# Optimization experiments

Hardware: AMD Instinct MI355X
Metric: run time of the kernel (lower is better)

## Reference

```python
import jax, jax.numpy as jnp
import numpy as np
import math

CHUNK = 64

def _linear(x, W, b):
    # torch nn.Linear: y = x @ W.T + b
    return jnp.einsum('bsd,ed->bse', x, W) + b

def setup_inputs() -> dict:
    key = jax.random.key(0)
    ks = jax.random.split(key, 10)
    B, S, D = 4, 4096, 512
    scale = 0.02
    inp = {
        'x': jax.random.normal(ks[0], (B, S, D), jnp.float32),
        'base_phases': jax.random.normal(ks[1], (S, D), jnp.float32) * math.pi,
        'Wk': jax.random.normal(ks[2], (D, D), jnp.float32) * scale,
        'bk': jnp.zeros((D,), jnp.float32),
        'Wv': jax.random.normal(ks[3], (D, D), jnp.float32) * scale,
        'bv': jnp.zeros((D,), jnp.float32),
        'Wq': jax.random.normal(ks[4], (D, D), jnp.float32) * scale,
        'bq': jnp.zeros((D,), jnp.float32),
        'Wkm': jax.random.normal(ks[5], (D, D), jnp.float32) * scale,
        'bkm': jnp.zeros((D,), jnp.float32),
        'Wqm': jax.random.normal(ks[6], (D, D), jnp.float32) * scale,
        'bqm': jnp.zeros((D,), jnp.float32),
        'mod_scale': jnp.ones((1,), jnp.float32) * 0.1,
        'ln_g': jnp.ones((D,), jnp.float32),
        'ln_b': jnp.zeros((D,), jnp.float32),
        'Wo': jax.random.normal(ks[7], (D, D), jnp.float32) * scale,
        'bo': jnp.zeros((D,), jnp.float32),
    }
    return inp

def reference(x, base_phases, Wk, bk, Wv, bv, Wq, bq, Wkm, bkm, Wqm, bqm, mod_scale, ln_g, ln_b, Wo, bo):
    B, S, D = x.shape
    bp = base_phases[:S][None]                      # [1,S,D]
    key = _linear(x, Wk, bk)
    value = _linear(x, Wv, bv)
    query = _linear(x, Wq, bq)
    key_phase = bp + _linear(key, Wkm, bkm) * mod_scale
    query_phase = bp + _linear(query, Wqm, bqm) * mod_scale
    bound_real = value * jnp.cos(key_phase)
    bound_imag = value * jnp.sin(key_phase)
    # chunked cumulative memory (S divisible by CHUNK -> no padding)
    nC = S // CHUNK
    br = bound_real.reshape(B, nC, CHUNK, D)
    bi = bound_imag.reshape(B, nC, CHUNK, D)
    qp = query_phase.reshape(B, nC, CHUNK, D)
    mem_real = jnp.cumsum(br, axis=2)
    mem_imag = jnp.cumsum(bi, axis=2)
    retrieved = (mem_real * jnp.cos(qp) + mem_imag * jnp.sin(qp)).reshape(B, S, D)
    retrieved = retrieved / math.sqrt(D)
    # LayerNorm + Linear (to_out)
    mu = jnp.mean(retrieved, axis=-1, keepdims=True)
    var = jnp.mean((retrieved - mu) ** 2, axis=-1, keepdims=True)
    normed = (retrieved - mu) / jnp.sqrt(var + 1e-5) * ln_g + ln_b
    out = _linear(normed, Wo, bo)
    return x + out
```

## Files before the change

### kernel.cpp

```cpp
#include <hip/hip_runtime.h>
#include <hip/hip_bf16.h>


typedef __attribute__((ext_vector_type(8))) short short8;
typedef __attribute__((ext_vector_type(4))) float f32x4;

#define M_TOK   16384
#define DIM     512
#define NCHUNK  64
#define RPAD    520

__device__ __forceinline__ void gll16(const void* g, void* l) {
  __builtin_amdgcn_global_load_lds(
      (const __attribute__((address_space(1))) unsigned int*)g,
      (__attribute__((address_space(3))) unsigned int*)l, 16, 0, 0);
}

__device__ __forceinline__ uint2 pack4bf(float4 v) {
  union { __hip_bfloat16 h[4]; uint2 u; } t;
  t.h[0] = __float2bfloat16(v.x);
  t.h[1] = __float2bfloat16(v.y);
  t.h[2] = __float2bfloat16(v.z);
  t.h[3] = __float2bfloat16(v.w);
  return t.u;
}

__device__ __forceinline__ unsigned int pack2bf(float a, float b) {
  union { __hip_bfloat16 h[2]; unsigned int u; } t;
  t.h[0] = __float2bfloat16(a);
  t.h[1] = __float2bfloat16(b);
  return t.u;
}

__device__ __forceinline__ float u2f(unsigned short u) {
  union { unsigned int i; float f; } t;
  t.i = (unsigned int)u << 16;
  return t.f;
}

__global__ __launch_bounds__(256) void prep_all(
    const float* __restrict__ x, __hip_bfloat16* __restrict__ x_bf,
    const float* __restrict__ Wv, const float* __restrict__ Wo,
    const float* __restrict__ bv,
    const float* __restrict__ Wkm, const float* __restrict__ Wqm,
    const float* __restrict__ Wk, const float* __restrict__ Wq,
    const float* __restrict__ bk, const float* __restrict__ bkm,
    const float* __restrict__ bq, const float* __restrict__ bqm,
    __hip_bfloat16* __restrict__ Wall, float* __restrict__ bc1,
    __hip_bfloat16* __restrict__ Wm_bf, __hip_bfloat16* __restrict__ WT_bf) {
  const int tid = threadIdx.x;
  if (blockIdx.x < 8192) {
    int i = blockIdx.x * 256 + tid;
    ((uint2*)x_bf)[i] = pack4bf(((const float4*)x)[i]);
    return;
  }
  const int b = blockIdx.x - 8192;
  if (b < 512) {
    int m = b >> 8;
    int idx = ((b & 255) * 256 + tid) * 4;
    const float* src = m ? Wo : Wv;
    __hip_bfloat16* dst = Wall + (m ? (size_t)1536 * 512 : 0);
    ((uint2*)dst)[idx >> 2] = pack4bf(*(const float4*)(src + idx));
    int t = b * 256 + tid;
    if (t < 512) bc1[t] = bv[t];
  } else if (b < 1024) {
    int bb = b - 512;
    int m = bb >> 8;
    int idx = ((bb & 255) * 256 + tid) * 4;
    const float* src = m ? Wqm : Wkm;
    ((uint2*)(Wm_bf + (size_t)m * 262144))[idx >> 2] =
        pack4bf(*(const float4*)(src + idx));
  } else if (b < 1152) {
    __shared__ float tile[64][65];
    int bb = b - 1024;
    int z = bb >> 6;
    int tl = bb & 63;
    int tr = tl >> 3, tc = tl & 7;
    const float* src = z ? Wq : Wk;
#pragma unroll
    for (int i = 0; i < 4; i++) {
      int r = (tid >> 4) + 16 * i;
      int c4 = (tid & 15) * 4;
      float4 v = *(const float4*)(src + (size_t)(tr * 64 + r) * 512 +
                                  tc * 64 + c4);
      tile[r][c4 + 0] = v.x;
      tile[r][c4 + 1] = v.y;
      tile[r][c4 + 2] = v.z;
      tile[r][c4 + 3] = v.w;
    }
    __syncthreads();
    int orow = tid >> 2;
    int seg = tid & 3;
    __hip_bfloat16* dst = WT_bf + (size_t)z * 262144 +
                          (size_t)(tc * 64 + orow) * 512 + tr * 64 + seg * 16;
#pragma unroll
    for (int q = 0; q < 4; q++) {
      float4 v;
      v.x = tile[seg * 16 + q * 4 + 0][orow];
      v.y = tile[seg * 16 + q * 4 + 1][orow];
      v.z = tile[seg * 16 + q * 4 + 2][orow];
      v.w = tile[seg * 16 + q * 4 + 3][orow];
      *(uint2*)(dst + q * 4) = pack4bf(v);
    }
  } else {
    int row = (b - 1152) * 4 + (tid >> 6);
    int lane = tid & 63;
    int z = row >> 9;
    int i = row & 511;
    const float* Wm = z ? Wqm : Wkm;
    const float* b0 = z ? bq : bk;
    const float* bm = z ? bqm : bkm;
    const float4* w4 = (const float4*)(Wm + (size_t)i * 512 + lane * 8);
    const float4* v4 = (const float4*)(b0 + lane * 8);
    float4 w0 = w4[0], w1 = w4[1], c0 = v4[0], c1 = v4[1];
    float acc = w0.x * c0.x + w0.y * c0.y + w0.z * c0.z + w0.w * c0.w +
                w1.x * c1.x + w1.y * c1.y + w1.z * c1.z + w1.w * c1.w;
#pragma unroll
    for (int off = 32; off; off >>= 1) acc += __shfl_xor(acc, off, 64);
    if (lane == 0) bc1[512 + z * 512 + i] = acc + bm[i];
  }
}

__global__ __launch_bounds__(256) void gemm_bt(
    const __hip_bfloat16* __restrict__ A, int lda,
    const __hip_bfloat16* __restrict__ Bt,
    const float* __restrict__ bias,
    __hip_bfloat16* __restrict__ Cout, int ldc) {
  constexpr int K = 512, BK = 32;
  __shared__ __align__(16) __hip_bfloat16 As[2][128 * BK];
  __shared__ __align__(16) __hip_bfloat16 Bs[2][128 * BK];

  const int tid  = threadIdx.x;
  const int lane = tid & 63;
  const int w    = tid >> 6;
  const int wm   = w >> 1;
  const int wn   = w & 1;
  const int lb = (blockIdx.x & 7) * 192 + (blockIdx.x >> 3);
  const int by = lb / 12;
  const int bx = lb - by * 12;
  const int m0 = by * 128;
  const int n0 = bx * 128;

  const int rS0    = (w * 2 + 0) * 16 + (lane >> 2);
  const int rS1    = (w * 2 + 1) * 16 + (lane >> 2);
  const int kInRow = (lane & 3) * 8;
  const __hip_bfloat16* gA0 = A + (size_t)(m0 + rS0) * lda + kInRow;
  const __hip_bfloat16* gA1 = A + (size_t)(m0 + rS1) * lda + kInRow;
  const __hip_bfloat16* gB0 = Bt + (size_t)(n0 + rS0) * K + kInRow;
  const __hip_bfloat16* gB1 = Bt + (size_t)(n0 + rS1) * K + kInRow;
  char* ldsA0 = (char*)&As[0][0] + (w * 2 + 0) * 1024;
  char* ldsA1 = (char*)&As[0][0] + (w * 2 + 1) * 1024;
  char* ldsB0 = (char*)&Bs[0][0] + (w * 2 + 0) * 1024;
  char* ldsB1 = (char*)&Bs[0][0] + (w * 2 + 1) * 1024;

  f32x4 acc[4][4] = {};

  const int rfA = lane & 15;
  const int rfK = (lane >> 4) * 8;

  for (int kt = 0; kt < K; kt += 2 * BK) {
    __syncthreads();
    gll16(gA0 + kt, ldsA0);
    gll16(gA1 + kt, ldsA1);
    gll16(gB0 + kt, ldsB0);
    gll16(gB1 + kt, ldsB1);
    gll16(gA0 + kt + BK, ldsA0 + 8192);
    gll16(gA1 + kt + BK, ldsA1 + 8192);
    gll16(gB0 + kt + BK, ldsB0 + 8192);
    gll16(gB1 + kt + BK, ldsB1 + 8192);
    __syncthreads();

#pragma unroll
    for (int h = 0; h < 2; h++) {
      const __hip_bfloat16* Ah = &As[h][0];
      const __hip_bfloat16* Bh = &Bs[h][0];
      short8 af[4], bfv[4];
#pragma unroll
      for (int i = 0; i < 4; i++)
        af[i] = *(const short8*)(Ah + (wm * 64 + i * 16 + rfA) * BK + rfK);
#pragma unroll
      for (int j = 0; j < 4; j++)
        bfv[j] = *(const short8*)(Bh + (wn * 64 + j * 16 + rfA) * BK + rfK);
#pragma unroll
      for (int i = 0; i < 4; i++)
#pragma unroll
        for (int j = 0; j < 4; j++)
          acc[i][j] = __builtin_amdgcn_mfma_f32_16x16x32_bf16(
              af[i], bfv[j], acc[i][j], 0, 0, 0);
    }
  }

  const int cq = lane >> 4;
#pragma unroll
  for (int i = 0; i < 4; i++) {
    int row = m0 + wm * 64 + i * 16 + cq * 4;
#pragma unroll
    for (int j = 0; j < 4; j++) {
      int col = n0 + wn * 64 + j * 16 + (lane & 15);
      float bz = bias[col];
#pragma unroll
      for (int r = 0; r < 4; r++) {
        float v = acc[i][j][r] + bz;
        Cout[(size_t)(row + r) * ldc + col] = __float2bfloat16(v);
      }
    }
  }
}

__global__ __launch_bounds__(256) void gemm_compose(
    const __hip_bfloat16* __restrict__ Wm_bf,
    const __hip_bfloat16* __restrict__ WT_bf,
    __hip_bfloat16* __restrict__ Wall) {
  constexpr int K = 512, BK = 32;
  const __hip_bfloat16* A  = Wm_bf + (size_t)blockIdx.z * 262144;
  const __hip_bfloat16* Bt = WT_bf + (size_t)blockIdx.z * 262144;
  __hip_bfloat16* C = Wall + (size_t)(512 + blockIdx.z * 512) * 512;
  __shared__ __align__(16) __hip_bfloat16 As[128 * BK];
  __shared__ __align__(16) __hip_bfloat16 Bs[128 * BK];

  const int tid  = threadIdx.x;
  const int lane = tid & 63;
  const int w    = tid >> 6;
  const int wm   = w >> 1;
  const int wn   = w & 1;
  const int m0   = blockIdx.y * 128;
  const int n0   = blockIdx.x * 128;

  const int rS0    = (w * 2 + 0) * 16 + (lane >> 2);
  const int rS1    = (w * 2 + 1) * 16 + (lane >> 2);
  const int kInRow = (lane & 3) * 8;
  const __hip_bfloat16* gA0 = A + (size_t)(m0 + rS0) * K + kInRow;
  const __hip_bfloat16* gA1 = A + (size_t)(m0 + rS1) * K + kInRow;
  const __hip_bfloat16* gB0 = Bt + (size_t)(n0 + rS0) * K + kInRow;
  const __hip_bfloat16* gB1 = Bt + (size_t)(n0 + rS1) * K + kInRow;
  char* ldsA0 = (char*)As + (w * 2 + 0) * 1024;
  char* ldsA1 = (char*)As + (w * 2 + 1) * 1024;
  char* ldsB0 = (char*)Bs + (w * 2 + 0) * 1024;
  char* ldsB1 = (char*)Bs + (w * 2 + 1) * 1024;

  f32x4 acc[4][4] = {};
  const int rfA = lane & 15;
  const int rfK = (lane >> 4) * 8;

  for (int kt = 0; kt < K; kt += BK) {
    __syncthreads();
    gll16(gA0 + kt, ldsA0);
    gll16(gA1 + kt, ldsA1);
    gll16(gB0 + kt, ldsB0);
    gll16(gB1 + kt, ldsB1);
    __syncthreads();

    short8 af[4], bf[4];
#pragma unroll
    for (int i = 0; i < 4; i++)
      af[i] = *(const short8*)(As + (wm * 64 + i * 16 + rfA) * BK + rfK);
#pragma unroll
    for (int j = 0; j < 4; j++)
      bf[j] = *(const short8*)(Bs + (wn * 64 + j * 16 + rfA) * BK + rfK);
#pragma unroll
    for (int i = 0; i < 4; i++)
#pragma unroll
      for (int j = 0; j < 4; j++)
        acc[i][j] = __builtin_amdgcn_mfma_f32_16x16x32_bf16(
            af[i], bf[j], acc[i][j], 0, 0, 0);
  }

  const int cq = lane >> 4;
#pragma unroll
  for (int i = 0; i < 4; i++) {
    int row = m0 + wm * 64 + i * 16 + cq * 4;
#pragma unroll
    for (int j = 0; j < 4; j++) {
      int col = n0 + wn * 64 + j * 16 + (lane & 15);
#pragma unroll
      for (int r = 0; r < 4; r++)
        C[(size_t)(row + r) * 512 + col] = __float2bfloat16(acc[i][j][r]);
    }
  }
}

__global__ __launch_bounds__(1024) void fused_pg(
    const __hip_bfloat16* __restrict__ VKQ,
    const float* __restrict__ bp,
    const float* __restrict__ mod_scale,
    const float* __restrict__ ln_g, const float* __restrict__ ln_b,
    const __hip_bfloat16* __restrict__ WoB,
    const float* __restrict__ bo,
    const float* __restrict__ x,
    float* __restrict__ out) {
  __shared__ __hip_bfloat16 R[64 * RPAD];
  __shared__ float Tr[3][512], Ti[3][512];
  const int tid    = threadIdx.x;
  const int seg    = tid >> 8;
  const int d0     = (tid & 255) * 2;
  const int blk    = blockIdx.x;
  const int token0 = blk * 64;
  const int sg0    = (blk & (NCHUNK - 1)) * 64;
  const float msc  = mod_scale[0];
  const float isd  = 0.044194173824159216f;

  float cqs0[16], sqs0[16], cqs1[16], sqs1[16];

  {
    const int r0 = seg * 16;
    float mr0 = 0.f, mi0 = 0.f, mr1 = 0.f, mi1 = 0.f;
    const __hip_bfloat16* vb = VKQ + (size_t)(token0 + r0) * 1536 + d0;
    const float* bb = bp + (size_t)(sg0 + r0) * 512 + d0;
#pragma unroll
    for (int s = 0; s < 16; ++s) {
      ushort2 v2  = *(const ushort2*)(vb + (size_t)s * 1536);
      ushort2 km2 = *(const ushort2*)(vb + (size_t)s * 1536 + 512);
      ushort2 qm2 = *(const ushort2*)(vb + (size_t)s * 1536 + 1024);
      float2 b2   = *(const float2*)(bb + (size_t)s * 512);
      float v0 = u2f((unsigned short)v2.x), v1 = u2f((unsigned short)v2.y);
      float kp0 = b2.x + u2f((unsigned short)km2.x) * msc;
      float kp1 = b2.y + u2f((unsigned short)km2.y) * msc;
      float qp0 = b2.x + u2f((unsigned short)qm2.x) * msc;
      float qp1 = b2.y + u2f((unsigned short)qm2.y) * msc;
      float sk0, ck0, sk1, ck1, sq0, cq0, sq1, cq1;
      __sincosf(kp0, &sk0, &ck0);
      __sincosf(kp1, &sk1, &ck1);
      __sincosf(qp0, &sq0, &cq0);
      __sincosf(qp1, &sq1, &cq1);
      mr0 += v0 * ck0; mi0 += v0 * sk0;
      mr1 += v1 * ck1; mi1 += v1 * sk1;
      cqs0[s] = cq0; sqs0[s] = sq0;
      cqs1[s] = cq1; sqs1[s] = sq1;
      float rr0 = (mr0 * cq0 + mi0 * sq0) * isd;
      float rr1 = (mr1 * cq1 + mi1 * sq1) * isd;
      *(unsigned int*)(&R[(r0 + s) * RPAD + d0]) = pack2bf(rr0, rr1);
    }
    if (seg < 3) {
      Tr[seg][d0] = mr0; Tr[seg][d0 + 1] = mr1;
      Ti[seg][d0] = mi0; Ti[seg][d0 + 1] = mi1;
    }
  }
  __syncthreads();

  if (seg) {
    float pr0 = Tr[0][d0],     pi0 = Ti[0][d0];
    float pr1 = Tr[0][d0 + 1], pi1 = Ti[0][d0 + 1];
    if (seg >= 2) {
      pr0 += Tr[1][d0];     pi0 += Ti[1][d0];
      pr1 += Tr[1][d0 + 1]; pi1 += Ti[1][d0 + 1];
    }
    if (seg == 3) {
      pr0 += Tr[2][d0];     pi0 += Ti[2][d0];
      pr1 += Tr[2][d0 + 1]; pi1 += Ti[2][d0 + 1];
    }
    pr0 *= isd; pi0 *= isd; pr1 *= isd; pi1 *= isd;
    const int r0 = seg * 16;
#pragma unroll
    for (int s = 0; s < 16; ++s) {
      unsigned int* p = (unsigned int*)(&R[(r0 + s) * RPAD + d0]);
      unsigned int old = *p;
      float a = u2f((unsigned short)(old & 0xffffu)) +
                pr0 * cqs0[s] + pi0 * sqs0[s];
      float b = u2f((unsigned short)(old >> 16)) +
                pr1 * cqs1[s] + pi1 * sqs1[s];
      *p = pack2bf(a, b);
    }
  }
  __syncthreads();

  const int lane = tid & 63;
  const int wv   = tid >> 6;
  float xv[4][2][4];

  {
    float gj[8], bj[8];
#pragma unroll
    for (int j = 0; j < 8; j++) {
      int col = lane + 64 * j;
      gj[j] = ln_g[col];
      bj[j] = ln_b[col];
    }
    {
      const int cq_ = lane >> 4;
      const int c0  = lane & 15;
#pragma unroll
      for (int i = 0; i < 4; i++)
#pragma unroll
        for (int j = 0; j < 2; j++)
#pragma unroll
          for (int r = 0; r < 4; r++)
            xv[i][j][r] = x[(size_t)(token0 + i * 16 + cq_ * 4 + r) * 512 +
                            wv * 32 + j * 16 + c0];
    }
    for (int rr = 0; rr < 4; ++rr) {
      int row = wv * 4 + rr;
      float vals[8], sum = 0.f, sq2 = 0.f;
#pragma unroll
      for (int j = 0; j < 8; j++) {
        float v = u2f(*(const unsigned short*)&R[row * RPAD + lane + 64 * j]);
        vals[j] = v;
        sum += v;
        sq2 += v * v;
      }
#pragma unroll
      for (int off = 32; off; off >>= 1) {
        sum += __shfl_xor(sum, off, 64);
        sq2 += __shfl_xor(sq2, off, 64);
      }
      float mu   = sum * (1.f / 512.f);
      float var  = sq2 * (1.f / 512.f) - mu * mu;
      float rstd = rsqrtf(var + 1e-5f);
#pragma unroll
      for (int j = 0; j < 8; j++) {
        float nv = (vals[j] - mu) * rstd * gj[j] + bj[j];
        R[row * RPAD + lane + 64 * j] = __float2bfloat16(nv);
      }
    }
  }
  __syncthreads();

  {
    const int rfA = lane & 15;
    const int rfK = (lane >> 4) * 8;
    f32x4 acc[4][2] = {};

    for (int kt = 0; kt < 512; kt += 32) {
      short8 af[4], bfv[2];
#pragma unroll
      for (int j = 0; j < 2; j++) {
        int col = wv * 32 + j * 16 + rfA;
        bfv[j] = *(const short8*)(WoB + (size_t)col * 512 + kt + rfK);
      }
#pragma unroll
      for (int i = 0; i < 4; i++)
        af[i] = *(const short8*)(R + (i * 16 + rfA) * RPAD + kt + rfK);
#pragma unroll
      for (int i = 0; i < 4; i++)
#pragma unroll
        for (int j = 0; j < 2; j++)
          acc[i][j] = __builtin_amdgcn_mfma_f32_16x16x32_bf16(
              af[i], bfv[j], acc[i][j], 0, 0, 0);
    }

    const int cq_ = lane >> 4;
    float bz[2];
#pragma unroll
    for (int j = 0; j < 2; j++) bz[j] = bo[wv * 32 + j * 16 + (lane & 15)];
#pragma unroll
    for (int i = 0; i < 4; i++) {
      int row = token0 + i * 16 + cq_ * 4;
#pragma unroll
      for (int j = 0; j < 2; j++) {
        int col = wv * 32 + j * 16 + (lane & 15);
#pragma unroll
        for (int r = 0; r < 4; r++) {
          size_t o = (size_t)(row + r) * 512 + col;
          out[o] = acc[i][j][r] + bz[j] + xv[i][j][r];
        }
      }
    }
  }
}

extern "C" void kernel_launch(void* const* d_in, const int* in_sizes, int n_in,
                              void* d_out, int out_size, void* d_ws,
                              size_t ws_size, hipStream_t stream) {
  const float* x    = (const float*)d_in[0];
  const float* bp   = (const float*)d_in[1];
  const float* Wk   = (const float*)d_in[2];
  const float* bk   = (const float*)d_in[3];
  const float* Wv   = (const float*)d_in[4];
  const float* bv   = (const float*)d_in[5];
  const float* Wq   = (const float*)d_in[6];
  const float* bq   = (const float*)d_in[7];
  const float* Wkm  = (const float*)d_in[8];
  const float* bkm  = (const float*)d_in[9];
  const float* Wqm  = (const float*)d_in[10];
  const float* bqm  = (const float*)d_in[11];
  const float* msc  = (const float*)d_in[12];
  const float* lng  = (const float*)d_in[13];
  const float* lnb  = (const float*)d_in[14];
  const float* Wo   = (const float*)d_in[15];
  const float* bo   = (const float*)d_in[16];
  float* out = (float*)d_out;

  char* ws = (char*)d_ws;
  __hip_bfloat16* x_bf  = (__hip_bfloat16*)ws;  ws += (size_t)M_TOK * DIM * 2;
  __hip_bfloat16* Wall  = (__hip_bfloat16*)ws;  ws += (size_t)2048 * 512 * 2;
  __hip_bfloat16* Wm_bf = (__hip_bfloat16*)ws;  ws += (size_t)2 * 262144 * 2;
  __hip_bfloat16* WT_bf = (__hip_bfloat16*)ws;  ws += (size_t)2 * 262144 * 2;
  float*          bc1   = (float*)ws;           ws += 1536 * 4;
  __hip_bfloat16* VKQ   = (__hip_bfloat16*)ws;  ws += (size_t)M_TOK * 1536 * 2;

  prep_all<<<9600, 256, 0, stream>>>(x, x_bf, Wv, Wo, bv, Wkm, Wqm, Wk, Wq,
                                     bk, bkm, bq, bqm, Wall, bc1, Wm_bf,
                                     WT_bf);
  gemm_compose<<<dim3(4, 4, 2), 256, 0, stream>>>(Wm_bf, WT_bf, Wall);
  gemm_bt<<<dim3(1536), 256, 0, stream>>>(x_bf, DIM, Wall, bc1, VKQ, 1536);
  fused_pg<<<256, 1024, 0, stream>>>(VKQ, bp, msc, lng, lnb,
                                     Wall + (size_t)1536 * 512, bo, x, out);
}
```

Measured before the change: 202.3 us.

## Split fused phasor/LayerNorm/out-proj kernel into separate scan and LN-GEMM kernels

Replaces the single 1024-thread-per-chunk fused kernel with two kernels. `phasor_scan` splits each 64-token chunk across two blocks by feature half, and uses two 32-row segments with a carry fix-up that recomputes the query sincos instead of holding it in registers. It writes the retrieved values to a bf16 global buffer that reuses the x_bf workspace. `ln_gemm` then processes 32-row tiles, doing LayerNorm with vectorised loads and an out-projection where each wave covers 128 output columns. The goal is more blocks, higher occupancy and less register pressure, at the cost of an extra kernel launch and a global round-trip of the intermediate.

```diff
diff --git a/kernel.cpp b/kernel.cpp
--- a/kernel.cpp
+++ b/kernel.cpp
@@ -8,7 +8,7 @@
 #define M_TOK   16384
 #define DIM     512
 #define NCHUNK  64
-#define RPAD    520
+#define NSPAD   520
 
 __device__ __forceinline__ void gll16(const void* g, void* l) {
   __builtin_amdgcn_global_load_lds(
@@ -279,44 +279,41 @@
   }
 }
 
-__global__ __launch_bounds__(1024) void fused_pg(
+__global__ __launch_bounds__(256, 4) void phasor_scan(
     const __hip_bfloat16* __restrict__ VKQ,
     const float* __restrict__ bp,
     const float* __restrict__ mod_scale,
-    const float* __restrict__ ln_g, const float* __restrict__ ln_b,
-    const __hip_bfloat16* __restrict__ WoB,
-    const float* __restrict__ bo,
-    const float* __restrict__ x,
-    float* __restrict__ out) {
-  __shared__ __hip_bfloat16 R[64 * RPAD];
-  __shared__ float Tr[3][512], Ti[3][512];
-  const int tid    = threadIdx.x;
-  const int seg    = tid >> 8;
-  const int d0     = (tid & 255) * 2;
-  const int blk    = blockIdx.x;
-  const int token0 = blk * 64;
-  const int sg0    = (blk & (NCHUNK - 1)) * 64;
+    __hip_bfloat16* __restrict__ Rg) {
+  __shared__ __hip_bfloat16 P[32][256];
+  __shared__ float Tr[256], Ti[256];
+  const int tid   = threadIdx.x;
+  const int seg   = tid >> 7;
+  const int dp    = tid & 127;
+  const int dloc  = dp * 2;
+  const int chunk = blockIdx.x >> 1;
+  const int half  = blockIdx.x & 1;
+  const int d0    = half * 256 + dloc;
+  const int token0 = chunk * 64;
+  const int sg0    = (chunk & (NCHUNK - 1)) * 64;
   const float msc  = mod_scale[0];
   const float isd  = 0.044194173824159216f;
 
-  float cqs0[16], sqs0[16], cqs1[16], sqs1[16];
-
   {
-    const int r0 = seg * 16;
+    const int r0 = seg * 32;
     float mr0 = 0.f, mi0 = 0.f, mr1 = 0.f, mi1 = 0.f;
     const __hip_bfloat16* vb = VKQ + (size_t)(token0 + r0) * 1536 + d0;
     const float* bb = bp + (size_t)(sg0 + r0) * 512 + d0;
-#pragma unroll
-    for (int s = 0; s < 16; ++s) {
+#pragma unroll 4
+    for (int s = 0; s < 32; ++s) {
       ushort2 v2  = *(const ushort2*)(vb + (size_t)s * 1536);
       ushort2 km2 = *(const ushort2*)(vb + (size_t)s * 1536 + 512);
       ushort2 qm2 = *(const ushort2*)(vb + (size_t)s * 1536 + 1024);
       float2 b2   = *(const float2*)(bb + (size_t)s * 512);
-      float v0 = u2f((unsigned short)v2.x), v1 = u2f((unsigned short)v2.y);
-      float kp0 = b2.x + u2f((unsigned short)km2.x) * msc;
-      float kp1 = b2.y + u2f((unsigned short)km2.y) * msc;
-      float qp0 = b2.x + u2f((unsigned short)qm2.x) * msc;
-      float qp1 = b2.y + u2f((unsigned short)qm2.y) * msc;
+      float v0 = u2f(v2.x), v1 = u2f(v2.y);
+      float kp0 = b2.x + u2f(km2.x) * msc;
+      float kp1 = b2.y + u2f(km2.y) * msc;
+      float qp0 = b2.x + u2f(qm2.x) * msc;
+      float qp1 = b2.y + u2f(qm2.y) * msc;
       float sk0, ck0, sk1, ck1, sq0, cq0, sq1, cq1;
       __sincosf(kp0, &sk0, &ck0);
       __sincosf(kp1, &sk1, &ck1);
@@ -324,75 +321,72 @@
       __sincosf(qp1, &sq1, &cq1);
       mr0 += v0 * ck0; mi0 += v0 * sk0;
       mr1 += v1 * ck1; mi1 += v1 * sk1;
-      cqs0[s] = cq0; sqs0[s] = sq0;
-      cqs1[s] = cq1; sqs1[s] = sq1;
       float rr0 = (mr0 * cq0 + mi0 * sq0) * isd;
       float rr1 = (mr1 * cq1 + mi1 * sq1) * isd;
-      *(unsigned int*)(&R[(r0 + s) * RPAD + d0]) = pack2bf(rr0, rr1);
-    }
-    if (seg < 3) {
-      Tr[seg][d0] = mr0; Tr[seg][d0 + 1] = mr1;
-      Ti[seg][d0] = mi0; Ti[seg][d0 + 1] = mi1;
+      unsigned int pw = pack2bf(rr0, rr1);
+      if (seg == 0)
+        *(unsigned int*)(Rg + (size_t)(token0 + s) * 512 + d0) = pw;
+      else
+        *(unsigned int*)(&P[s][dloc]) = pw;
+    }
+    if (seg == 0) {
+      Tr[dloc] = mr0; Tr[dloc + 1] = mr1;
+      Ti[dloc] = mi0; Ti[dloc + 1] = mi1;
     }
   }
   __syncthreads();
 
-  if (seg) {
-    float pr0 = Tr[0][d0],     pi0 = Ti[0][d0];
-    float pr1 = Tr[0][d0 + 1], pi1 = Ti[0][d0 + 1];
-    if (seg >= 2) {
-      pr0 += Tr[1][d0];     pi0 += Ti[1][d0];
-      pr1 += Tr[1][d0 + 1]; pi1 += Ti[1][d0 + 1];
-    }
-    if (seg == 3) {
-      pr0 += Tr[2][d0];     pi0 += Ti[2][d0];
-      pr1 += Tr[2][d0 + 1]; pi1 += Ti[2][d0 + 1];
-    }
-    pr0 *= isd; pi0 *= isd; pr1 *= isd; pi1 *= isd;
-    const int r0 = seg * 16;
-#pragma unroll
+  {
+    const float pr0 = Tr[dloc] * isd,     pi0 = Ti[dloc] * isd;
+    const float pr1 = Tr[dloc + 1] * isd, pi1 = Ti[dloc + 1] * isd;
+    const int rf = 32 + seg * 16;
+    const __hip_bfloat16* qb = VKQ + (size_t)(token0 + rf) * 1536 + 1024 + d0;
+    const float* bb = bp + (size_t)(sg0 + rf) * 512 + d0;
+#pragma unroll 4
     for (int s = 0; s < 16; ++s) {
-      unsigned int* p = (unsigned int*)(&R[(r0 + s) * RPAD + d0]);
-      unsigned int old = *p;
-      float a = u2f((unsigned short)(old & 0xffffu)) +
-                pr0 * cqs0[s] + pi0 * sqs0[s];
-      float b = u2f((unsigned short)(old >> 16)) +
-                pr1 * cqs1[s] + pi1 * sqs1[s];
-      *p = pack2bf(a, b);
-    }
-  }
-  __syncthreads();
-
+      ushort2 qm2 = *(const ushort2*)(qb + (size_t)s * 1536);
+      float2 b2   = *(const float2*)(bb + (size_t)s * 512);
+      float qp0 = b2.x + u2f(qm2.x) * msc;
+      float qp1 = b2.y + u2f(qm2.y) * msc;
+      float sq0, cq0, sq1, cq1;
+      __sincosf(qp0, &sq0, &cq0);
+      __sincosf(qp1, &sq1, &cq1);
+      unsigned int old = *(unsigned int*)(&P[rf - 32 + s][dloc]);
+      float a = u2f((unsigned short)(old & 0xffffu)) + pr0 * cq0 + pi0 * sq0;
+      float b = u2f((unsigned short)(old >> 16))     + pr1 * cq1 + pi1 * sq1;
+      *(unsigned int*)(Rg + (size_t)(token0 + rf + s) * 512 + d0) =
+          pack2bf(a, b);
+    }
+  }
+}
+
+__global__ __launch_bounds__(256, 4) void ln_gemm(
+    const __hip_bfloat16* __restrict__ Rg,
+    const float* __restrict__ ln_g, const float* __restrict__ ln_b,
+    const __hip_bfloat16* __restrict__ WoB,
+    const float* __restrict__ bo,
+    const float* __restrict__ x,
+    float* __restrict__ out) {
+  __shared__ __align__(16) __hip_bfloat16 Ns[32 * NSPAD];
+  const int tid  = threadIdx.x;
   const int lane = tid & 63;
   const int wv   = tid >> 6;
-  float xv[4][2][4];
+  const int row0 = blockIdx.x * 32;
 
   {
-    float gj[8], bj[8];
-#pragma unroll
-    for (int j = 0; j < 8; j++) {
-      int col = lane + 64 * j;
-      gj[j] = ln_g[col];
-      bj[j] = ln_b[col];
-    }
-    {
-      const int cq_ = lane >> 4;
-      const int c0  = lane & 15;
-#pragma unroll
-      for (int i = 0; i < 4; i++)
-#pragma unroll
-        for (int j = 0; j < 2; j++)
-#pragma unroll
-          for (int r = 0; r < 4; r++)
-            xv[i][j][r] = x[(size_t)(token0 + i * 16 + cq_ * 4 + r) * 512 +
-                            wv * 32 + j * 16 + c0];
-    }
-    for (int rr = 0; rr < 4; ++rr) {
-      int row = wv * 4 + rr;
+    float4 g0 = *(const float4*)(ln_g + lane * 8);
+    float4 g1 = *(const float4*)(ln_g + lane * 8 + 4);
+    float4 c0 = *(const float4*)(ln_b + lane * 8);
+    float4 c1 = *(const float4*)(ln_b + lane * 8 + 4);
+    float gj[8] = {g0.x, g0.y, g0.z, g0.w, g1.x, g1.y, g1.z, g1.w};
+    float bj[8] = {c0.x, c0.y, c0.z, c0.w, c1.x, c1.y, c1.z, c1.w};
+    for (int rr = 0; rr < 8; ++rr) {
+      int row = wv * 8 + rr;
+      short8 v8 = *(const short8*)(Rg + (size_t)(row0 + row) * 512 + lane * 8);
       float vals[8], sum = 0.f, sq2 = 0.f;
 #pragma unroll
       for (int j = 0; j < 8; j++) {
-        float v = u2f(*(const unsigned short*)&R[row * RPAD + lane + 64 * j]);
+        float v = u2f((unsigned short)v8[j]);
         vals[j] = v;
         sum += v;
         sq2 += v * v;
@@ -405,11 +399,14 @@
       float mu   = sum * (1.f / 512.f);
       float var  = sq2 * (1.f / 512.f) - mu * mu;
       float rstd = rsqrtf(var + 1e-5f);
+      short8 n8;
 #pragma unroll
       for (int j = 0; j < 8; j++) {
-        float nv = (vals[j] - mu) * rstd * gj[j] + bj[j];
-        R[row * RPAD + lane + 64 * j] = __float2bfloat16(nv);
-      }
+        union { __hip_bfloat16 h; unsigned short s; } cv;
+        cv.h = __float2bfloat16((vals[j] - mu) * rstd * gj[j] + bj[j]);
+        n8[j] = (short)cv.s;
+      }
+      *(short8*)(Ns + row * NSPAD + lane * 8) = n8;
     }
   }
   __syncthreads();
@@ -417,40 +414,36 @@
   {
     const int rfA = lane & 15;
     const int rfK = (lane >> 4) * 8;
-    f32x4 acc[4][2] = {};
+    f32x4 acc[2][8] = {};
 
     for (int kt = 0; kt < 512; kt += 32) {
-      short8 af[4], bfv[2];
-#pragma unroll
-      for (int j = 0; j < 2; j++) {
-        int col = wv * 32 + j * 16 + rfA;
-        bfv[j] = *(const short8*)(WoB + (size_t)col * 512 + kt + rfK);
-      }
-#pragma unroll
-      for (int i = 0; i < 4; i++)
-        af[i] = *(const short8*)(R + (i * 16 + rfA) * RPAD + kt + rfK);
-#pragma unroll
-      for (int i = 0; i < 4; i++)
-#pragma unroll
-        for (int j = 0; j < 2; j++)
-          acc[i][j] = __builtin_amdgcn_mfma_f32_16x16x32_bf16(
-              af[i], bfv[j], acc[i][j], 0, 0, 0);
-    }
-
-    const int cq_ = lane >> 4;
-    float bz[2];
-#pragma unroll
-    for (int j = 0; j < 2; j++) bz[j] = bo[wv * 32 + j * 16 + (lane & 15)];
-#pragma unroll
-    for (int i = 0; i < 4; i++) {
-      int row = token0 + i * 16 + cq_ * 4;
-#pragma unroll
-      for (int j = 0; j < 2; j++) {
-        int col = wv * 32 + j * 16 + (lane & 15);
+      short8 af0 = *(const short8*)(Ns + (rfA) * NSPAD + kt + rfK);
+      short8 af1 = *(const short8*)(Ns + (16 + rfA) * NSPAD + kt + rfK);
+#pragma unroll
+      for (int j = 0; j < 8; ++j) {
+        short8 bf8 = *(const short8*)(
+            WoB + (size_t)(wv * 128 + j * 16 + rfA) * 512 + kt + rfK);
+        acc[0][j] = __builtin_amdgcn_mfma_f32_16x16x32_bf16(
+            af0, bf8, acc[0][j], 0, 0, 0);
+        acc[1][j] = __builtin_amdgcn_mfma_f32_16x16x32_bf16(
+            af1, bf8, acc[1][j], 0, 0, 0);
+      }
+    }
+
+    const int cq = lane >> 4;
+    float bz[8];
+#pragma unroll
+    for (int j = 0; j < 8; j++) bz[j] = bo[wv * 128 + j * 16 + (lane & 15)];
+#pragma unroll
+    for (int i = 0; i < 2; i++) {
+      int row = row0 + i * 16 + cq * 4;
+#pragma unroll
+      for (int j = 0; j < 8; j++) {
+        int col = wv * 128 + j * 16 + (lane & 15);
 #pragma unroll
         for (int r = 0; r < 4; r++) {
           size_t o = (size_t)(row + r) * 512 + col;
-          out[o] = acc[i][j][r] + bz[j] + xv[i][j][r];
+          out[o] = acc[i][j][r] + bz[j] + x[o];
         }
       }
     }
@@ -486,12 +479,14 @@
   __hip_bfloat16* WT_bf = (__hip_bfloat16*)ws;  ws += (size_t)2 * 262144 * 2;
   float*          bc1   = (float*)ws;           ws += 1536 * 4;
   __hip_bfloat16* VKQ   = (__hip_bfloat16*)ws;  ws += (size_t)M_TOK * 1536 * 2;
+  __hip_bfloat16* Rg = x_bf;
 
   prep_all<<<9600, 256, 0, stream>>>(x, x_bf, Wv, Wo, bv, Wkm, Wqm, Wk, Wq,
                                      bk, bkm, bq, bqm, Wall, bc1, Wm_bf,
                                      WT_bf);
   gemm_compose<<<dim3(4, 4, 2), 256, 0, stream>>>(Wm_bf, WT_bf, Wall);
   gemm_bt<<<dim3(1536), 256, 0, stream>>>(x_bf, DIM, Wall, bc1, VKQ, 1536);
-  fused_pg<<<256, 1024, 0, stream>>>(VKQ, bp, msc, lng, lnb,
-                                     Wall + (size_t)1536 * 512, bo, x, out);
-}
+  phasor_scan<<<512, 256, 0, stream>>>(VKQ, bp, msc, Rg);
+  ln_gemm<<<512, 256, 0, stream>>>(Rg, lng, lnb, Wall + (size_t)1536 * 512,
+                                   bo, x, out);
+}
```

Result: slower. 251.6 us (+24.4%).
